# Kernel optimization log

Measured on AMD Instinct MI355X. Metric: run time of the kernel, lower is better.

The kernel has to match this reference:

```python
import jax, jax.numpy as jnp
import numpy as np

B, S, HID, NH, MAX_TOKENS = 2, 2048, 2048, 16, 2048
HD = HID // NH

def rotate_half(x):
    x1, x2 = x[..., :x.shape[-1] // 2], x[..., x.shape[-1] // 2:]
    return jnp.concatenate((-x2, x1), axis=-1)

def rope_tables():
    inv_freq = 1.0 / (10000.0 ** (jnp.arange(0, HD, 2, dtype=jnp.float32) / HD))
    t = jnp.arange(MAX_TOKENS, dtype=jnp.float32)
    freqs = jnp.outer(t, inv_freq)                       # [T, HD/2]
    emb = jnp.concatenate((freqs, freqs), axis=-1)       # [T, HD]
    return jnp.cos(emb), jnp.sin(emb)

def setup_inputs() -> dict:
    key = jax.random.key(0)
    ks = jax.random.split(key, 5)
    hidden_states = jax.random.normal(ks[0], (B, S, HID), dtype=jnp.float32)
    # additive causal mask [B, 1, S, S]: 0 on/below diag, large negative above
    neg = jnp.finfo(jnp.float32).min
    causal = jnp.where(jnp.tril(jnp.ones((S, S), dtype=bool)), 0.0, neg)
    attention_mask = jnp.broadcast_to(causal[None, None], (B, 1, S, S)).astype(jnp.float32)
    position_ids = jnp.broadcast_to(jnp.arange(S, dtype=jnp.int32), (B, S))
    scale = 1.0 / np.sqrt(HID)
    Wq = jax.random.normal(ks[1], (HID, HID), dtype=jnp.float32) * scale
    Wk = jax.random.normal(ks[2], (HID, HID), dtype=jnp.float32) * scale
    Wv = jax.random.normal(ks[3], (HID, HID), dtype=jnp.float32) * scale
    Wo = jax.random.normal(ks[4], (HID, HID), dtype=jnp.float32) * scale
    return {"hidden_states": hidden_states, "attention_mask": attention_mask,
            "position_ids": position_ids, "Wq": Wq, "Wk": Wk, "Wv": Wv, "Wo": Wo}

def reference(hidden_states, attention_mask, position_ids, Wq, Wk, Wv, Wo):
    b, s, _ = hidden_states.shape
    def proj(W):  # torch Linear: x @ W.T -> [b, H, s, hd]
        return (hidden_states @ W.T).reshape(b, s, NH, HD).transpose(0, 2, 1, 3)
    q, k, v = proj(Wq), proj(Wk), proj(Wv)
    cos_t, sin_t = rope_tables()
    cos = cos_t[position_ids][:, None]   # [b, 1, s, hd]
    sin = sin_t[position_ids][:, None]
    q = q * cos + rotate_half(q) * sin
    k = k * cos + rotate_half(k) * sin
    scores = jnp.einsum('bhqd,bhkd->bhqk', q, k) / np.sqrt(HD)
    scores = jnp.maximum(scores + attention_mask, jnp.finfo(scores.dtype).min)
    attn = jax.nn.softmax(scores.astype(jnp.float32), axis=-1).astype(q.dtype)
    out = jnp.einsum('bhqk,bhkd->bhqd', attn, v)
    out = out.transpose(0, 2, 1, 3).reshape(b, s, HID)
    return out @ Wo.T
```

## Files before the change

### kernel.cpp

```cpp
#include <hip/hip_runtime.h>

#define B_   2
#define S_   2048
#define HID_ 2048
#define NH_  16
#define HD_  128
#define MAXTOK_ 2048

typedef float  f32x4  __attribute__((ext_vector_type(4)));
typedef __bf16 bf16x8 __attribute__((ext_vector_type(8)));

__device__ __forceinline__ unsigned short f2bf(float f) {
  union { float fv; unsigned u; } v; v.fv = f;
  unsigned r = v.u + 0x7FFFu + ((v.u >> 16) & 1u);
  return (unsigned short)(r >> 16);
}
__device__ __forceinline__ float bf2f(unsigned short h) {
  union { unsigned u; float fv; } v; v.u = ((unsigned)h) << 16;
  return v.fv;
}

__device__ __forceinline__ void gload16(const void* g, void* lds) {
  __builtin_amdgcn_global_load_lds(
      (const __attribute__((address_space(1))) void*)g,
      (__attribute__((address_space(3))) void*)lds, 16, 0, 0);
}

#define H4_ (B_ * S_ * HID_ / 4)
#define W4_ (HID_ * HID_ / 4)
__global__ void cast_all(const float* __restrict__ h,  const float* __restrict__ wq,
                         const float* __restrict__ wk, const float* __restrict__ wv,
                         const float* __restrict__ wo,
                         unsigned short* __restrict__ xb,  unsigned short* __restrict__ wqb,
                         unsigned short* __restrict__ wkb, unsigned short* __restrict__ wvb,
                         unsigned short* __restrict__ wob) {
  const int total = H4_ + 4 * W4_;
  int i = blockIdx.x * blockDim.x + threadIdx.x;
  int stride = gridDim.x * blockDim.x;
  for (; i < total; i += stride) {
    const float* src; unsigned short* dst; int j;
    if (i < H4_) { src = h; dst = xb; j = i; }
    else {
      int k = i - H4_, wsel = k >> 20;
      j = k & (W4_ - 1);
      src = (wsel == 0) ? wq : (wsel == 1) ? wk : (wsel == 2) ? wv : wo;
      dst = (wsel == 0) ? wqb : (wsel == 1) ? wkb : (wsel == 2) ? wvb : wob;
    }
    float4 v = ((const float4*)src)[j];
    ushort4 o;
    o.x = f2bf(v.x); o.y = f2bf(v.y); o.z = f2bf(v.z); o.w = f2bf(v.w);
    ((ushort4*)dst)[j] = o;
  }
}


__global__ __launch_bounds__(256, 2)
void gemm_qkv(const unsigned short* __restrict__ A,
              const unsigned short* __restrict__ Bw,
              unsigned short* __restrict__ Qb,
              unsigned short* __restrict__ Kb,
              unsigned short* __restrict__ Vtmp) {
  const int K = HID_;
  __shared__ __align__(16) unsigned short As[128 * 32];
  __shared__ __align__(16) unsigned short Bs[128 * 32];
  const int tid = threadIdx.x, lane = tid & 63, w = tid >> 6;
  const int n0 = blockIdx.x * 128, m0 = blockIdx.y * 128;
  const int wm = (w & 1) * 64, wn = (w >> 1) * 64;
  const int rowq = lane & 15;
  const int koff = (lane >> 4) * 8;
  const int lr0 = (lane >> 4) * 4;

  f32x4 acc[4][4];
  for (int i = 0; i < 4; ++i)
    for (int j = 0; j < 4; ++j)
      for (int r = 0; r < 4; ++r) acc[i][j][r] = 0.f;

  for (int k0 = 0; k0 < K; k0 += 32) {
    __syncthreads();
    for (int c = 0; c < 2; ++c) {
      int chunk = (w * 2 + c) * 64 + lane;
      int row = chunk >> 2, cc = chunk & 3;
      gload16(A + (size_t)(m0 + row) * K + k0 + cc * 8, As + (w * 2 + c) * 512);
      gload16(Bw + (size_t)(n0 + row) * K + k0 + cc * 8, Bs + (w * 2 + c) * 512);
    }
    __syncthreads();
    bf16x8 af[4], bfv[4];
    for (int i = 0; i < 4; ++i) {
      af[i]  = *(const bf16x8*)&As[(wm + i * 16 + rowq) * 32 + koff];
      bfv[i] = *(const bf16x8*)&Bs[(wn + i * 16 + rowq) * 32 + koff];
    }
    for (int mi = 0; mi < 4; ++mi)
      for (int ni = 0; ni < 4; ++ni)
        acc[mi][ni] = __builtin_amdgcn_mfma_f32_16x16x32_bf16(af[mi], bfv[ni], acc[mi][ni], 0, 0, 0);
  }

  for (int mi = 0; mi < 4; ++mi)
    for (int ni = 0; ni < 4; ++ni)
      for (int r = 0; r < 4; ++r) {
        int r_ = m0 + wm + mi * 16 + lr0 + r;
        int c_ = n0 + wn + ni * 16 + rowq;
        float v = acc[mi][ni][r];
        int b = r_ >> 11, s = r_ & 2047;
        int proj = c_ >> 11, cin = c_ & 2047;
        if (proj == 2) {
          Vtmp[(size_t)(b * S_ + s) * HID_ + cin] = f2bf(v);
        } else {
          int hh = cin >> 7, d = cin & 127;
          unsigned short* dst = (proj == 0) ? Qb : Kb;
          dst[(((size_t)(b * NH_ + hh) * S_ + s) * HD_) + d] = f2bf(v);
        }
      }
}

__global__ __launch_bounds__(256, 2)
void gemm_out(const unsigned short* __restrict__ A,
              const unsigned short* __restrict__ Bw,
              float* __restrict__ Cout) {
  const int N = HID_, K = HID_;
  __shared__ __align__(16) unsigned short As[128 * 32];
  __shared__ __align__(16) unsigned short Bs[128 * 32];
  const int tid = threadIdx.x, lane = tid & 63, w = tid >> 6;
  const int n0 = blockIdx.x * 128, m0 = blockIdx.y * 128;
  const int wm = (w & 1) * 64, wn = (w >> 1) * 64;
  const int rowq = lane & 15;
  const int koff = (lane >> 4) * 8;
  const int lr0 = (lane >> 4) * 4;

  f32x4 acc[4][4];
  for (int i = 0; i < 4; ++i)
    for (int j = 0; j < 4; ++j)
      for (int r = 0; r < 4; ++r) acc[i][j][r] = 0.f;

  for (int k0 = 0; k0 < K; k0 += 32) {
    __syncthreads();
    for (int c = 0; c < 2; ++c) {
      int chunk = (w * 2 + c) * 64 + lane;
      int row = chunk >> 2, cc = chunk & 3;
      gload16(A + (size_t)(m0 + row) * K + k0 + cc * 8, As + (w * 2 + c) * 512);
      gload16(Bw + (size_t)(n0 + row) * K + k0 + cc * 8, Bs + (w * 2 + c) * 512);
    }
    __syncthreads();
    bf16x8 af[4], bfv[4];
    for (int i = 0; i < 4; ++i) {
      af[i]  = *(const bf16x8*)&As[(wm + i * 16 + rowq) * 32 + koff];
      bfv[i] = *(const bf16x8*)&Bs[(wn + i * 16 + rowq) * 32 + koff];
    }
    for (int mi = 0; mi < 4; ++mi)
      for (int ni = 0; ni < 4; ++ni)
        acc[mi][ni] = __builtin_amdgcn_mfma_f32_16x16x32_bf16(af[mi], bfv[ni], acc[mi][ni], 0, 0, 0);
  }

  for (int mi = 0; mi < 4; ++mi)
    for (int ni = 0; ni < 4; ++ni)
      for (int r = 0; r < 4; ++r) {
        int r_ = m0 + wm + mi * 16 + lr0 + r;
        int c_ = n0 + wn + ni * 16 + rowq;
        Cout[(size_t)r_ * N + c_] = acc[mi][ni][r];
      }
}

__global__ void rope_table(float2* __restrict__ tbl) {
  int i = blockIdx.x * blockDim.x + threadIdx.x;
  if (i >= MAXTOK_ * 64) return;
  int p = i >> 6, d = i & 63;
  float f = __expf(-(float)d * (9.210340371976184f / 64.f));
  float sn, cs;
  __sincosf((float)p * f, &sn, &cs);
  tbl[i] = make_float2(cs, sn);
}

#define QSCALE_ 0.12751744f
__global__ __launch_bounds__(256)
void rope_apply(unsigned short* __restrict__ Qb, unsigned short* __restrict__ Kb,
                const int* __restrict__ pos_ids, const float2* __restrict__ tbl) {
  int i = blockIdx.x * blockDim.x + threadIdx.x;
  int d = i & 63, bhs = i >> 6;
  int s = bhs & (S_ - 1);
  int b = bhs >> 15;
  int p = pos_ids[b * S_ + s];
  float2 cssn = tbl[p * 64 + d];
  size_t base = (size_t)bhs * HD_;
  {
    float x1 = bf2f(Qb[base + d]), x2 = bf2f(Qb[base + d + 64]);
    Qb[base + d]      = f2bf((x1 * cssn.x - x2 * cssn.y) * QSCALE_);
    Qb[base + d + 64] = f2bf((x2 * cssn.x + x1 * cssn.y) * QSCALE_);
  }
  {
    float x1 = bf2f(Kb[base + d]), x2 = bf2f(Kb[base + d + 64]);
    Kb[base + d]      = f2bf(x1 * cssn.x - x2 * cssn.y);
    Kb[base + d + 64] = f2bf(x2 * cssn.x + x1 * cssn.y);
  }
}

__global__ __launch_bounds__(256)
void transpose_v(const unsigned short* __restrict__ Vin,
                 unsigned short* __restrict__ Vt) {
  __shared__ unsigned short t[64 * 66];
  const int s0 = blockIdx.x * 64, d0 = blockIdx.y * 64, bh = blockIdx.z;
  const int b = bh >> 4, h = bh & 15;
  for (int it = 0; it < 16; ++it) {
    int lin = it * 256 + threadIdx.x;
    int sl = lin >> 6, dl = lin & 63;
    t[sl * 66 + dl] = Vin[(size_t)(b * S_ + s0 + sl) * HID_ + h * HD_ + d0 + dl];
  }
  __syncthreads();
  for (int it = 0; it < 16; ++it) {
    int lin = it * 256 + threadIdx.x;
    int dl = lin >> 6, sl = lin & 63;
    Vt[((size_t)bh * HD_ + d0 + dl) * S_ + s0 + sl] = t[sl * 66 + dl];
  }
}

#define KS_LD 136
#define VS_LD 72
#define PS_LD 72
__global__ __launch_bounds__(256, 2)
void attn_fused(const unsigned short* __restrict__ Qb,
                const unsigned short* __restrict__ Kb,
                const unsigned short* __restrict__ Vt,
                unsigned short* __restrict__ Ob) {
  __shared__ __align__(16) unsigned short Ks[64 * KS_LD];
  __shared__ __align__(16) unsigned short Vts[128 * VS_LD];
  __shared__ __align__(16) unsigned short Ps[4 * 16 * PS_LD];

  const int tid = threadIdx.x, lane = tid & 63, w = tid >> 6;
  const int bh = blockIdx.x;
  const int qt = (gridDim.y - 1) - blockIdx.y;
  const int q0 = qt * 64;
  const int b = bh >> 4, h = bh & 15;
  const int rowq = lane & 15;
  const int koff = (lane >> 4) * 8;
  const int lr0 = (lane >> 4) * 4;
  const size_t qkbase = (size_t)bh * (S_ * HD_);
  const size_t vbase  = (size_t)bh * (HD_ * S_);

  bf16x8 qf0, qf1, qf2, qf3;
  {
    const unsigned short* qrow = Qb + qkbase + (size_t)(q0 + w * 16 + rowq) * HD_;
    qf0 = *(const bf16x8*)(qrow + 0 * 32 + koff);
    qf1 = *(const bf16x8*)(qrow + 1 * 32 + koff);
    qf2 = *(const bf16x8*)(qrow + 2 * 32 + koff);
    qf3 = *(const bf16x8*)(qrow + 3 * 32 + koff);
  }

  const int krow = tid >> 4, kcol = (tid & 15) * 8;
  const int vrow = tid >> 3, vcol = (tid & 7) * 8;
  const unsigned short* kptr = Kb + qkbase + (size_t)krow * HD_ + kcol;
  const unsigned short* vptr = Vt + vbase + (size_t)vrow * S_ + vcol;

  f32x4 oacc[8];
  for (int i = 0; i < 8; ++i)
    for (int r = 0; r < 4; ++r) oacc[i][r] = 0.f;
  float m_r[4] = {-3e38f, -3e38f, -3e38f, -3e38f};
  float l_r[4] = {0.f, 0.f, 0.f, 0.f};

  const int nkt = qt + 1;

  float4 k0, k1, k2, k3, v0, v1, v2, v3;
  k0 = *(const float4*)(kptr + 0 * 16 * HD_);
  k1 = *(const float4*)(kptr + 1 * 16 * HD_);
  k2 = *(const float4*)(kptr + 2 * 16 * HD_);
  k3 = *(const float4*)(kptr + 3 * 16 * HD_);
  v0 = *(const float4*)(vptr + 0 * 32 * S_);
  v1 = *(const float4*)(vptr + 1 * 32 * S_);
  v2 = *(const float4*)(vptr + 2 * 32 * S_);
  v3 = *(const float4*)(vptr + 3 * 32 * S_);

  for (int kt = 0; kt < nkt; ++kt) {
    __syncthreads();
    *(float4*)&Ks[(krow + 0 * 16) * KS_LD + kcol] = k0;
    *(float4*)&Ks[(krow + 1 * 16) * KS_LD + kcol] = k1;
    *(float4*)&Ks[(krow + 2 * 16) * KS_LD + kcol] = k2;
    *(float4*)&Ks[(krow + 3 * 16) * KS_LD + kcol] = k3;
    *(float4*)&Vts[(vrow + 0 * 32) * VS_LD + vcol] = v0;
    *(float4*)&Vts[(vrow + 1 * 32) * VS_LD + vcol] = v1;
    *(float4*)&Vts[(vrow + 2 * 32) * VS_LD + vcol] = v2;
    *(float4*)&Vts[(vrow + 3 * 32) * VS_LD + vcol] = v3;
    if (kt + 1 < nkt) {
      const unsigned short* kp = kptr + (size_t)(kt + 1) * 64 * HD_;
      k0 = *(const float4*)(kp + 0 * 16 * HD_);
      k1 = *(const float4*)(kp + 1 * 16 * HD_);
      k2 = *(const float4*)(kp + 2 * 16 * HD_);
      k3 = *(const float4*)(kp + 3 * 16 * HD_);
    }
    __syncthreads();

    f32x4 sacc[4];
    for (int n = 0; n < 4; ++n)
      for (int r = 0; r < 4; ++r) sacc[n][r] = 0.f;
#pragma unroll
    for (int n = 0; n < 4; ++n) {
      const unsigned short* krow_p = &Ks[(n * 16 + rowq) * KS_LD + koff];
      sacc[n] = __builtin_amdgcn_mfma_f32_16x16x32_bf16(qf0, *(const bf16x8*)(krow_p + 0 * 32), sacc[n], 0, 0, 0);
      sacc[n] = __builtin_amdgcn_mfma_f32_16x16x32_bf16(qf1, *(const bf16x8*)(krow_p + 1 * 32), sacc[n], 0, 0, 0);
      sacc[n] = __builtin_amdgcn_mfma_f32_16x16x32_bf16(qf2, *(const bf16x8*)(krow_p + 2 * 32), sacc[n], 0, 0, 0);
      sacc[n] = __builtin_amdgcn_mfma_f32_16x16x32_bf16(qf3, *(const bf16x8*)(krow_p + 3 * 32), sacc[n], 0, 0, 0);
    }

    float tmax[4] = {-3e38f, -3e38f, -3e38f, -3e38f};
    if (kt == qt) {
      for (int n = 0; n < 4; ++n) {
        int col = n * 16 + rowq;
        for (int r = 0; r < 4; ++r) {
          int row = w * 16 + lr0 + r;
          float x = (col <= row) ? sacc[n][r] : -1e30f;
          sacc[n][r] = x;
          tmax[r] = fmaxf(tmax[r], x);
        }
      }
    } else {
      for (int n = 0; n < 4; ++n)
        for (int r = 0; r < 4; ++r)
          tmax[r] = fmaxf(tmax[r], sacc[n][r]);
    }
    for (int off = 1; off < 16; off <<= 1)
      for (int r = 0; r < 4; ++r) tmax[r] = fmaxf(tmax[r], __shfl_xor(tmax[r], off));
    float alpha[4];
    for (int r = 0; r < 4; ++r) {
      float mn = fmaxf(m_r[r], tmax[r]);
      alpha[r] = __builtin_amdgcn_exp2f(m_r[r] - mn);
      m_r[r] = mn;
    }
    float rs[4] = {0.f, 0.f, 0.f, 0.f};
    for (int n = 0; n < 4; ++n)
      for (int r = 0; r < 4; ++r) {
        float p = __builtin_amdgcn_exp2f(sacc[n][r] - m_r[r]);
        sacc[n][r] = p;
        rs[r] += p;
      }
    for (int off = 1; off < 16; off <<= 1)
      for (int r = 0; r < 4; ++r) rs[r] += __shfl_xor(rs[r], off);
    for (int r = 0; r < 4; ++r) l_r[r] = l_r[r] * alpha[r] + rs[r];
    for (int nd = 0; nd < 8; ++nd)
      for (int r = 0; r < 4; ++r) oacc[nd][r] *= alpha[r];

    if (kt + 1 < nkt) {
      const unsigned short* vp = vptr + (size_t)(kt + 1) * 64;
      v0 = *(const float4*)(vp + 0 * 32 * S_);
      v1 = *(const float4*)(vp + 1 * 32 * S_);
      v2 = *(const float4*)(vp + 2 * 32 * S_);
      v3 = *(const float4*)(vp + 3 * 32 * S_);
    }

    unsigned short* pw = &Ps[w * 16 * PS_LD];
    for (int n = 0; n < 4; ++n)
      for (int r = 0; r < 4; ++r)
        pw[(lr0 + r) * PS_LD + n * 16 + rowq] = f2bf(sacc[n][r]);

#pragma unroll
    for (int t2 = 0; t2 < 2; ++t2) {
      bf16x8 pa = *(const bf16x8*)&pw[rowq * PS_LD + t2 * 32 + koff];
      for (int nd = 0; nd < 8; ++nd) {
        bf16x8 vb = *(const bf16x8*)&Vts[(nd * 16 + rowq) * VS_LD + t2 * 32 + koff];
        oacc[nd] = __builtin_amdgcn_mfma_f32_16x16x32_bf16(pa, vb, oacc[nd], 0, 0, 0);
      }
    }
  }

  float linv[4];
  for (int r = 0; r < 4; ++r) linv[r] = __builtin_amdgcn_rcpf(l_r[r]);
  for (int nd = 0; nd < 8; ++nd) {
    int col = h * HD_ + nd * 16 + rowq;
    for (int r = 0; r < 4; ++r) {
      int row = q0 + w * 16 + lr0 + r;
      Ob[(size_t)(b * S_ + row) * HID_ + col] = f2bf(oacc[nd][r] * linv[r]);
    }
  }
}

extern "C" void kernel_launch(void* const* d_in, const int* in_sizes, int n_in,
                              void* d_out, int out_size, void* d_ws, size_t ws_size,
                              hipStream_t stream) {
  (void)in_sizes; (void)n_in; (void)out_size; (void)ws_size;
  const float* hidden = (const float*)d_in[0];
  const int* pos = (const int*)d_in[2];
  const float* Wq = (const float*)d_in[3];
  const float* Wk = (const float*)d_in[4];
  const float* Wv = (const float*)d_in[5];
  const float* Wo = (const float*)d_in[6];
  float* out = (float*)d_out;

  char* ws = (char*)d_ws;
  unsigned short* Xb   = (unsigned short*)(ws);
  unsigned short* Wqb  = (unsigned short*)(ws + 16777216);
  unsigned short* Wkb  = (unsigned short*)(ws + 25165824);
  unsigned short* Wvb  = (unsigned short*)(ws + 33554432);
  unsigned short* Wob  = (unsigned short*)(ws + 41943040);
  unsigned short* Qb   = (unsigned short*)(ws + 50331648);
  unsigned short* Kb   = (unsigned short*)(ws + 67108864);
  unsigned short* Vtmp = (unsigned short*)(ws + 83886080);
  unsigned short* Vtb  = (unsigned short*)(ws + 100663296);
  unsigned short* Ob   = Xb;
  float2* tbl          = (float2*)ws;

  cast_all<<<2048, 256, 0, stream>>>(hidden, Wq, Wk, Wv, Wo, Xb, Wqb, Wkb, Wvb, Wob);

  dim3 gq(3 * HID_ / 128, (B_ * S_) / 128);
  gemm_qkv<<<gq, 256, 0, stream>>>(Xb, Wqb, Qb, Kb, Vtmp);

  rope_table<<<(MAXTOK_ * 64) / 256, 256, 0, stream>>>(tbl);
  rope_apply<<<(B_ * NH_ * S_ * 64) / 256, 256, 0, stream>>>(Qb, Kb, pos, tbl);

  dim3 tg(S_ / 64, HD_ / 64, B_ * NH_);
  transpose_v<<<tg, 256, 0, stream>>>(Vtmp, Vtb);

  dim3 ag(B_ * NH_, S_ / 64);
  attn_fused<<<ag, 256, 0, stream>>>(Qb, Kb, Vtb, Ob);

  dim3 go(HID_ / 128, (B_ * S_) / 128);
  gemm_out<<<go, 256, 0, stream>>>(Ob, Wob, out);
}
```

Baseline: 443.0 us.

## Rewrite QKV GEMM with 256x256 tiles, double-buffered swizzled LDS, and interleaved prefetch

The QKV projection GEMM moves from 128x128 tiles with BK=32 and 256 threads to 256x256 tiles with BK=64 and 512 threads. LDS is double-buffered with an XOR swizzle to avoid bank conflicts. Global-to-LDS loads for the next K tile are interleaved with four MFMA quadrants, using manual s_barrier, vmcnt waits and setprio. The aim is to hide memory latency and raise MFMA reuse per loaded byte. In exchange it uses 128KB of LDS per block and fewer blocks, which lowers occupancy and leaves a wave-quantization tail on the 24x16 grid.

New measurement: 440.8 us. No clear change (-0.5%).

```diff
diff --git a/kernel.cpp b/kernel.cpp
--- a/kernel.cpp
+++ b/kernel.cpp
@@ -53,49 +53,145 @@
   }
 }
 
-
-__global__ __launch_bounds__(256, 2)
+#define QKV_STG(gp, lp, rb) gload16((gp) + (size_t)(rb) * 2048, (lp) + (rb) * 64)
+
+#define QKV_LOADA(MH) do { \
+  _Pragma("unroll") \
+  for (int mi_ = 0; mi_ < 4; ++mi_) { \
+    const char* rp_ = (const char*)Acur + (size_t)((wm + (MH) * 64 + mi_ * 16 + rowq) * 128); \
+    af[mi_][0] = *(const bf16x8*)(rp_ + cb0); \
+    af[mi_][1] = *(const bf16x8*)(rp_ + cb1); \
+  } } while (0)
+
+#define QKV_LOADB(NP) do { \
+  _Pragma("unroll") \
+  for (int ni_ = 0; ni_ < 2; ++ni_) { \
+    const char* rp_ = (const char*)Bcur + (size_t)((wn + (NP) * 32 + ni_ * 16 + rowq) * 128); \
+    bfr[ni_][0] = *(const bf16x8*)(rp_ + cb0); \
+    bfr[ni_][1] = *(const bf16x8*)(rp_ + cb1); \
+  } } while (0)
+
+#define QKV_MFMA(MH, NP) do { \
+  _Pragma("unroll") \
+  for (int mi_ = 0; mi_ < 4; ++mi_) { \
+    _Pragma("unroll") \
+    for (int ni_ = 0; ni_ < 2; ++ni_) { \
+      f32x4 c_ = acc[(MH) * 4 + mi_][(NP) * 2 + ni_]; \
+      c_ = __builtin_amdgcn_mfma_f32_16x16x32_bf16(af[mi_][0], bfr[ni_][0], c_, 0, 0, 0); \
+      c_ = __builtin_amdgcn_mfma_f32_16x16x32_bf16(af[mi_][1], bfr[ni_][1], c_, 0, 0, 0); \
+      acc[(MH) * 4 + mi_][(NP) * 2 + ni_] = c_; \
+    } } } while (0)
+
+#define QKV_BAR    asm volatile("s_barrier" ::: "memory")
+#define QKV_VMC2   asm volatile("s_waitcnt vmcnt(2)" ::: "memory")
+#define QKV_VMC0   asm volatile("s_waitcnt vmcnt(0)" ::: "memory")
+
+__global__ __launch_bounds__(512, 2)
 void gemm_qkv(const unsigned short* __restrict__ A,
               const unsigned short* __restrict__ Bw,
               unsigned short* __restrict__ Qb,
               unsigned short* __restrict__ Kb,
               unsigned short* __restrict__ Vtmp) {
   const int K = HID_;
-  __shared__ __align__(16) unsigned short As[128 * 32];
-  __shared__ __align__(16) unsigned short Bs[128 * 32];
+  const int NT = K / 64;
+  __shared__ __align__(16) unsigned short As[2][256 * 64];
+  __shared__ __align__(16) unsigned short Bs[2][256 * 64];
+
   const int tid = threadIdx.x, lane = tid & 63, w = tid >> 6;
-  const int n0 = blockIdx.x * 128, m0 = blockIdx.y * 128;
-  const int wm = (w & 1) * 64, wn = (w >> 1) * 64;
-  const int rowq = lane & 15;
-  const int koff = (lane >> 4) * 8;
-  const int lr0 = (lane >> 4) * 4;
-
-  f32x4 acc[4][4];
-  for (int i = 0; i < 4; ++i)
+  const int n0 = blockIdx.x * 256, m0 = blockIdx.y * 256;
+  const int wm = (w >> 2) * 128, wn = (w & 3) * 64;
+  const int rowq = lane & 15, klane = lane >> 4;
+  const int sw  = ((rowq >> 2) & 1) << 5;
+  const int cb0 = (klane * 16) ^ sw;
+  const int cb1 = (64 + klane * 16) ^ sw;
+  const int srow = tid >> 3;
+  const int dc8  = (tid & 7) * 8;
+  const int scol = (((tid & 7) * 16) ^ (((srow >> 2) & 1) << 5)) >> 1;
+
+  const unsigned short* Ag = A  + (size_t)(m0 + srow) * K + scol;
+  const unsigned short* Bg = Bw + (size_t)(n0 + srow) * K + scol;
+
+  f32x4 acc[8][4];
+#pragma unroll
+  for (int i = 0; i < 8; ++i)
+#pragma unroll
     for (int j = 0; j < 4; ++j)
+#pragma unroll
       for (int r = 0; r < 4; ++r) acc[i][j][r] = 0.f;
 
-  for (int k0 = 0; k0 < K; k0 += 32) {
-    __syncthreads();
-    for (int c = 0; c < 2; ++c) {
-      int chunk = (w * 2 + c) * 64 + lane;
-      int row = chunk >> 2, cc = chunk & 3;
-      gload16(A + (size_t)(m0 + row) * K + k0 + cc * 8, As + (w * 2 + c) * 512);
-      gload16(Bw + (size_t)(n0 + row) * K + k0 + cc * 8, Bs + (w * 2 + c) * 512);
-    }
-    __syncthreads();
-    bf16x8 af[4], bfv[4];
-    for (int i = 0; i < 4; ++i) {
-      af[i]  = *(const bf16x8*)&As[(wm + i * 16 + rowq) * 32 + koff];
-      bfv[i] = *(const bf16x8*)&Bs[(wn + i * 16 + rowq) * 32 + koff];
-    }
-    for (int mi = 0; mi < 4; ++mi)
-      for (int ni = 0; ni < 4; ++ni)
-        acc[mi][ni] = __builtin_amdgcn_mfma_f32_16x16x32_bf16(af[mi], bfv[ni], acc[mi][ni], 0, 0, 0);
-  }
-
-  for (int mi = 0; mi < 4; ++mi)
+  bf16x8 af[4][2], bfr[2][2];
+
+  {
+    unsigned short* Al = (unsigned short*)&As[0][0] + srow * 64 + dc8;
+    unsigned short* Bl = (unsigned short*)&Bs[0][0] + srow * 64 + dc8;
+    QKV_STG(Bg, Bl, 0); QKV_STG(Bg, Bl, 64); QKV_STG(Bg, Bl, 128); QKV_STG(Bg, Bl, 192);
+    QKV_STG(Ag, Al, 0); QKV_STG(Ag, Al, 128); QKV_STG(Ag, Al, 64); QKV_STG(Ag, Al, 192);
+  }
+  QKV_VMC2;
+  QKV_BAR;
+
+  const unsigned short* Acur = &As[0][0];
+  const unsigned short* Bcur = &Bs[0][0];
+  unsigned short* Anx = (unsigned short*)&As[1][0];
+  unsigned short* Bnx = (unsigned short*)&Bs[1][0];
+
+  for (int t = 0; t < NT - 1; ++t) {
+    const int kn = (t + 1) * 64;
+    const unsigned short* Agk = Ag + kn;
+    const unsigned short* Bgk = Bg + kn;
+    unsigned short* Al = Anx + srow * 64 + dc8;
+    unsigned short* Bl = Bnx + srow * 64 + dc8;
+
+    QKV_LOADA(0); QKV_LOADB(0);
+    QKV_STG(Bgk, Bl, 0); QKV_STG(Bgk, Bl, 64);
+    QKV_BAR;
+    __builtin_amdgcn_s_setprio(1); QKV_MFMA(0, 0); __builtin_amdgcn_s_setprio(0);
+    QKV_VMC2;
+    QKV_BAR;
+    QKV_LOADA(1);
+    QKV_STG(Bgk, Bl, 128); QKV_STG(Bgk, Bl, 192);
+    QKV_BAR;
+    __builtin_amdgcn_s_setprio(1); QKV_MFMA(1, 0); __builtin_amdgcn_s_setprio(0);
+    QKV_BAR;
+    QKV_LOADB(1);
+    QKV_STG(Agk, Al, 0); QKV_STG(Agk, Al, 128);
+    QKV_BAR;
+    __builtin_amdgcn_s_setprio(1); QKV_MFMA(1, 1); __builtin_amdgcn_s_setprio(0);
+    QKV_BAR;
+    QKV_LOADA(0);
+    QKV_STG(Agk, Al, 64); QKV_STG(Agk, Al, 192);
+    QKV_BAR;
+    __builtin_amdgcn_s_setprio(1); QKV_MFMA(0, 1); __builtin_amdgcn_s_setprio(0);
+    QKV_VMC2;
+    QKV_BAR;
+
+    { const unsigned short* tp = Acur; Acur = Anx; Anx = (unsigned short*)tp; }
+    { const unsigned short* tp = Bcur; Bcur = Bnx; Bnx = (unsigned short*)tp; }
+  }
+
+  QKV_LOADA(0); QKV_LOADB(0);
+  QKV_BAR;
+  __builtin_amdgcn_s_setprio(1); QKV_MFMA(0, 0); __builtin_amdgcn_s_setprio(0);
+  QKV_VMC0;
+  QKV_BAR;
+  QKV_LOADA(1);
+  QKV_BAR;
+  __builtin_amdgcn_s_setprio(1); QKV_MFMA(1, 0); __builtin_amdgcn_s_setprio(0);
+  QKV_BAR;
+  QKV_LOADB(1);
+  QKV_BAR;
+  __builtin_amdgcn_s_setprio(1); QKV_MFMA(1, 1); __builtin_amdgcn_s_setprio(0);
+  QKV_BAR;
+  QKV_LOADA(0);
+  QKV_BAR;
+  __builtin_amdgcn_s_setprio(1); QKV_MFMA(0, 1); __builtin_amdgcn_s_setprio(0);
+
+  const int lr0 = klane * 4;
+#pragma unroll
+  for (int mi = 0; mi < 8; ++mi)
+#pragma unroll
     for (int ni = 0; ni < 4; ++ni)
+#pragma unroll
       for (int r = 0; r < 4; ++r) {
         int r_ = m0 + wm + mi * 16 + lr0 + r;
         int c_ = n0 + wn + ni * 16 + rowq;
@@ -395,8 +491,8 @@
 
   cast_all<<<2048, 256, 0, stream>>>(hidden, Wq, Wk, Wv, Wo, Xb, Wqb, Wkb, Wvb, Wob);
 
-  dim3 gq(3 * HID_ / 128, (B_ * S_) / 128);
-  gemm_qkv<<<gq, 256, 0, stream>>>(Xb, Wqb, Qb, Kb, Vtmp);
+  dim3 gq(3 * HID_ / 256, (B_ * S_) / 256);
+  gemm_qkv<<<gq, 512, 0, stream>>>(Xb, Wqb, Qb, Kb, Vtmp);
 
   rope_table<<<(MAXTOK_ * 64) / 256, 256, 0, stream>>>(tbl);
   rope_apply<<<(B_ * NH_ * S_ * 64) / 256, 256, 0, stream>>>(Qb, Kb, pos, tbl);
```
